# Kernel optimization log

Hardware: AMD Instinct MI355X
Metric: run time of the kernel (lower is better)

The kernel has to match this reference:

```python
import jax, jax.numpy as jnp
import numpy as np


def _inside_mask(points, boxes3d):
    # points: (B, N, 3); boxes3d: (B, M, 7) = (cx, cy, cz_bottom, dx, dy, dz, rz)
    cx, cy, cz, dx, dy, dz, rz = [boxes3d[..., i] for i in range(7)]
    cz = cz + dz * 0.5  # bottom-center -> geometric center (mmcv convention)
    # shift into box frame: (B, M, N)
    sx = points[:, None, :, 0] - cx[..., None]
    sy = points[:, None, :, 1] - cy[..., None]
    sz = points[:, None, :, 2] - cz[..., None]
    cosa = jnp.cos(-rz)[..., None]
    sina = jnp.sin(-rz)[..., None]
    lx = sx * cosa - sy * sina
    ly = sx * sina + sy * cosa
    return (
        (jnp.abs(lx) < dx[..., None] * 0.5)
        & (jnp.abs(ly) < dy[..., None] * 0.5)
        & (jnp.abs(sz) <= dz[..., None] * 0.5)
    )


def setup_inputs() -> dict:
    key = jax.random.key(0)
    k1, k2, k3 = jax.random.split(key, 3)
    B, N, M, C = 4, 16384, 128, 128
    points = jax.random.uniform(k1, (B, N, 3), dtype=jnp.float32)
    point_features = jax.random.normal(k2, (B, N, C), dtype=jnp.float32)
    boxes3d = jax.random.uniform(k3, (B, M, 7), dtype=jnp.float32)
    return {
        "points": points,
        "point_features": point_features,
        "boxes3d": boxes3d,
        "num_sampled_points": 512,
    }


def reference(points, point_features, boxes3d, num_sampled_points):
    S = num_sampled_points
    mask = _inside_mask(points, boxes3d)            # (B, M, N) bool
    cnt = mask.sum(axis=-1)                          # (B, M)
    # stable sort brings inside-point indices first, in original order
    order = jnp.argsort((~mask).astype(jnp.int32), axis=-1, stable=True)  # (B, M, N)
    cnt_safe = jnp.maximum(cnt, 1)
    # CUDA kernel: sample index k maps to k % cnt (== k when k < cnt)
    sample_pos = jnp.arange(S, dtype=cnt.dtype)[None, None, :] % cnt_safe[..., None]
    idx = jnp.take_along_axis(order, sample_pos, axis=-1)  # (B, M, S)
    gathered_pts = jnp.take_along_axis(points[:, None], idx[..., None], axis=2)          # (B, M, S, 3)
    gathered_feat = jnp.take_along_axis(point_features[:, None], idx[..., None], axis=2)  # (B, M, S, C)
    pooled = jnp.concatenate([gathered_pts, gathered_feat], axis=-1)  # (B, M, S, 3+C)
    nonempty = (cnt > 0)
    pooled = pooled * nonempty[..., None, None].astype(pooled.dtype)
    empty_flag = (~nonempty).astype(jnp.int32)
    return pooled, empty_flag
```

## Files before the change

kernel.cpp:

```cpp
#include <hip/hip_runtime.h>
#include <hip/hip_bf16.h>

#define BB   4
#define NN   16384
#define MM   128
#define CC   128
#define SS   512
#define CH   (CC + 3)
#define BM   (BB * MM)
#define WAVES 8
#define CHUNK (NN / WAVES)

__global__ __launch_bounds__(512)
void box_sample_kernel(const float* __restrict__ points,
                       const float* __restrict__ boxes,
                       int*  __restrict__ idx_ws,
                       int*  __restrict__ cnt_ws,
                       float* __restrict__ flag_out)
{
    const int box  = blockIdx.x;
    const int b    = box >> 7;
    const int lane = threadIdx.x & 63;
    const int w    = threadIdx.x >> 6;

    const float* P  = points + (size_t)b * NN * 3;
    const float* bx = boxes  + (size_t)box * 7;

    const float cx = bx[0], cy = bx[1], cz = bx[2];
    const float dx = bx[3], dy = bx[4], dz = bx[5], rz = bx[6];

    const float  czc = cz + dz * 0.5f;
    const float  hz  = dz * 0.5f;
    const double ca  = cos(-(double)rz);
    const double sa  = sin(-(double)rz);
    const double hx  = (double)dx * 0.5;
    const double hy  = (double)dy * 0.5;

    __shared__ int s_part[WAVES][SS];
    __shared__ int s_cnt[WAVES];
    __shared__ int s_idx[SS];

    int cnt = 0;
    const int pbase = w * CHUNK;
    for (int i0 = 0; i0 < CHUNK; i0 += 256) {
        float px[4], py[4], pz[4];
        #pragma unroll
        for (int u = 0; u < 4; ++u) {
            const int i = pbase + i0 + u * 64 + lane;
            px[u] = P[i * 3 + 0];
            py[u] = P[i * 3 + 1];
            pz[u] = P[i * 3 + 2];
        }
        #pragma unroll
        for (int u = 0; u < 4; ++u) {
            const double sx = (double)px[u] - (double)cx;
            const double sy = (double)py[u] - (double)cy;
            const float  szf = pz[u] - czc;
            const double lx = sx * ca - sy * sa;
            const double ly = sx * sa + sy * ca;
            const bool inside = (fabs(lx) < hx) && (fabs(ly) < hy) && (fabsf(szf) <= hz);
            const unsigned long long mask = __ballot(inside);
            const int pos = cnt + __popcll(mask & ((1ull << lane) - 1ull));
            if (inside && pos < SS) s_part[w][pos] = pbase + i0 + u * 64 + lane;
            cnt += __popcll(mask);
        }
    }
    if (lane == 0) s_cnt[w] = cnt;
    __syncthreads();

    int c[WAVES], off[WAVES];
    int total = 0;
    #pragma unroll
    for (int q = 0; q < WAVES; ++q) { c[q] = s_cnt[q]; off[q] = total; total += c[q]; }

    for (int k = threadIdx.x; k < SS; k += 512) {
        int v = 0;
        #pragma unroll
        for (int q = 0; q < WAVES; ++q) {
            const int r = k - off[q];
            if (r >= 0 && r < c[q]) v = s_part[q][r];
        }
        s_idx[k] = v;
    }
    __syncthreads();

    if (total > 0 && total < SS) {
        for (int k = total + threadIdx.x; k < SS; k += 512)
            s_idx[k] = s_idx[k % total];
        __syncthreads();
    }

    int* dst = idx_ws + (size_t)box * SS;
    for (int k = threadIdx.x; k < SS; k += 512) dst[k] = s_idx[k];
    if (threadIdx.x == 0) {
        cnt_ws[box]   = total;
        flag_out[box] = (total == 0) ? 1.0f : 0.0f;
    }
}

__global__ __launch_bounds__(256)
void gather_kernel(const float* __restrict__ points,
                   const float* __restrict__ feats,
                   const int*   __restrict__ idx_ws,
                   const int*   __restrict__ cnt_ws,
                   float* __restrict__ out)
{
    const int box   = blockIdx.x;
    const int chunk = blockIdx.y;
    const int b     = box >> 7;
    const int tid   = threadIdx.x;
    const int hw    = tid >> 5;
    const int j     = tid & 31;

    __shared__ int   s_idx[32];
    __shared__ float s_scale;
    __shared__ __align__(16) float s_buf[32 * CH];

    if (tid < 32) s_idx[tid] = idx_ws[(size_t)box * SS + chunk * 32 + tid];
    if (tid == 0) s_scale = (cnt_ws[box] > 0) ? 1.0f : 0.0f;
    __syncthreads();
    const float scale = s_scale;

    const float4* F4 = (const float4*)(feats + (size_t)b * NN * CC);
    const float*  Pb = points + (size_t)b * NN * 3;

    #pragma unroll
    for (int s = 0; s < 4; ++s) {
        const int k   = hw + s * 8;
        const int idx = s_idx[k];
        const float4 v = F4[idx * 32 + j];
        const int base = k * CH + 3 + 4 * j;
        s_buf[base + 0] = v.x * scale;
        s_buf[base + 1] = v.y * scale;
        s_buf[base + 2] = v.z * scale;
        s_buf[base + 3] = v.w * scale;
        if (j < 3) s_buf[k * CH + j] = Pb[idx * 3 + j] * scale;
    }
    __syncthreads();

    const float4* src4 = (const float4*)s_buf;
    float4* dst4 = (float4*)(out + (size_t)box * SS * CH + (size_t)chunk * 32 * CH);
    #pragma unroll
    for (int s = 0; s < 4; ++s) dst4[s * 256 + tid] = src4[s * 256 + tid];
    if (tid < 24) dst4[1024 + tid] = src4[1024 + tid];
}

extern "C" void kernel_launch(void* const* d_in, const int* in_sizes, int n_in,
                              void* d_out, int out_size, void* d_ws, size_t ws_size,
                              hipStream_t stream) {
    const float* points = (const float*)d_in[0];
    const float* feats  = (const float*)d_in[1];
    const float* boxes  = (const float*)d_in[2];

    int*  idx_ws = (int*)d_ws;
    int*  cnt_ws = idx_ws + (size_t)BM * SS;
    float* out      = (float*)d_out;
    float* flag_out = out + (size_t)BM * SS * CH;

    box_sample_kernel<<<BM, 512, 0, stream>>>(points, boxes, idx_ws, cnt_ws, flag_out);
    dim3 ggrid(BM, SS / 32);
    gather_kernel<<<ggrid, 256, 0, stream>>>(points, feats, idx_ws, cnt_ws, out);
}
```

Baseline: 197.7 us.

## Fuse box sampling and feature gather into one kernel per box

Merges the point-in-box sampling kernel and the gather kernel into a single kernel with one 512-thread block per box. The sampled indices stay in shared memory and the shared buffer is reused for staging 64 samples per iteration, so the index workspace round trip and the second launch go away. Output is written with nontemporal stores. In exchange the gather now runs with only 512 blocks and serialised per-box loops instead of 8192 blocks, which may reduce memory-level parallelism.

```diff
diff --git a/kernel.cpp b/kernel.cpp
--- a/kernel.cpp
+++ b/kernel.cpp
@@ -11,17 +11,20 @@
 #define WAVES 8
 #define CHUNK (NN / WAVES)
 
+typedef float vfloat4 __attribute__((ext_vector_type(4)));
+
 __global__ __launch_bounds__(512)
-void box_sample_kernel(const float* __restrict__ points,
-                       const float* __restrict__ boxes,
-                       int*  __restrict__ idx_ws,
-                       int*  __restrict__ cnt_ws,
-                       float* __restrict__ flag_out)
+void roipool_fused_kernel(const float* __restrict__ points,
+                          const float* __restrict__ feats,
+                          const float* __restrict__ boxes,
+                          float* __restrict__ out,
+                          float* __restrict__ flag_out)
 {
     const int box  = blockIdx.x;
     const int b    = box >> 7;
-    const int lane = threadIdx.x & 63;
-    const int w    = threadIdx.x >> 6;
+    const int tid  = threadIdx.x;
+    const int lane = tid & 63;
+    const int w    = tid >> 6;
 
     const float* P  = points + (size_t)b * NN * 3;
     const float* bx = boxes  + (size_t)box * 7;
@@ -36,9 +39,10 @@
     const double hx  = (double)dx * 0.5;
     const double hy  = (double)dy * 0.5;
 
-    __shared__ int s_part[WAVES][SS];
+    __shared__ __align__(16) float s_buf[64 * CH];
+    __shared__ int s_idx[SS];
     __shared__ int s_cnt[WAVES];
-    __shared__ int s_idx[SS];
+    int (*s_part)[SS] = (int (*)[SS])s_buf;
 
     int cnt = 0;
     const int pbase = w * CHUNK;
@@ -73,7 +77,7 @@
     #pragma unroll
     for (int q = 0; q < WAVES; ++q) { c[q] = s_cnt[q]; off[q] = total; total += c[q]; }
 
-    for (int k = threadIdx.x; k < SS; k += 512) {
+    for (int k = tid; k < SS; k += 512) {
         int v = 0;
         #pragma unroll
         for (int q = 0; q < WAVES; ++q) {
@@ -85,64 +89,44 @@
     __syncthreads();
 
     if (total > 0 && total < SS) {
-        for (int k = total + threadIdx.x; k < SS; k += 512)
+        for (int k = total + tid; k < SS; k += 512)
             s_idx[k] = s_idx[k % total];
-        __syncthreads();
-    }
-
-    int* dst = idx_ws + (size_t)box * SS;
-    for (int k = threadIdx.x; k < SS; k += 512) dst[k] = s_idx[k];
-    if (threadIdx.x == 0) {
-        cnt_ws[box]   = total;
-        flag_out[box] = (total == 0) ? 1.0f : 0.0f;
-    }
-}
-
-__global__ __launch_bounds__(256)
-void gather_kernel(const float* __restrict__ points,
-                   const float* __restrict__ feats,
-                   const int*   __restrict__ idx_ws,
-                   const int*   __restrict__ cnt_ws,
-                   float* __restrict__ out)
-{
-    const int box   = blockIdx.x;
-    const int chunk = blockIdx.y;
-    const int b     = box >> 7;
-    const int tid   = threadIdx.x;
-    const int hw    = tid >> 5;
-    const int j     = tid & 31;
-
-    __shared__ int   s_idx[32];
-    __shared__ float s_scale;
-    __shared__ __align__(16) float s_buf[32 * CH];
-
-    if (tid < 32) s_idx[tid] = idx_ws[(size_t)box * SS + chunk * 32 + tid];
-    if (tid == 0) s_scale = (cnt_ws[box] > 0) ? 1.0f : 0.0f;
-    __syncthreads();
-    const float scale = s_scale;
-
-    const float4* F4 = (const float4*)(feats + (size_t)b * NN * CC);
-    const float*  Pb = points + (size_t)b * NN * 3;
-
-    #pragma unroll
-    for (int s = 0; s < 4; ++s) {
-        const int k   = hw + s * 8;
-        const int idx = s_idx[k];
-        const float4 v = F4[idx * 32 + j];
-        const int base = k * CH + 3 + 4 * j;
-        s_buf[base + 0] = v.x * scale;
-        s_buf[base + 1] = v.y * scale;
-        s_buf[base + 2] = v.z * scale;
-        s_buf[base + 3] = v.w * scale;
-        if (j < 3) s_buf[k * CH + j] = Pb[idx * 3 + j] * scale;
     }
     __syncthreads();
 
-    const float4* src4 = (const float4*)s_buf;
-    float4* dst4 = (float4*)(out + (size_t)box * SS * CH + (size_t)chunk * 32 * CH);
-    #pragma unroll
-    for (int s = 0; s < 4; ++s) dst4[s * 256 + tid] = src4[s * 256 + tid];
-    if (tid < 24) dst4[1024 + tid] = src4[1024 + tid];
+    const float scale = (total > 0) ? 1.0f : 0.0f;
+    if (tid == 0) flag_out[box] = (total == 0) ? 1.0f : 0.0f;
+
+    const float4* F4 = (const float4*)(feats + (size_t)b * NN * CC);
+    const float*  Pb = P;
+    const int hw = tid >> 5;
+    const int j  = tid & 31;
+    float* outbox = out + (size_t)box * SS * CH;
+
+    for (int g = 0; g < 8; ++g) {
+        #pragma unroll
+        for (int s = 0; s < 4; ++s) {
+            const int kl  = s * 16 + hw;
+            const int idx = s_idx[g * 64 + kl];
+            const float4 v = F4[idx * 32 + j];
+            const int base = kl * CH + 3 + 4 * j;
+            s_buf[base + 0] = v.x * scale;
+            s_buf[base + 1] = v.y * scale;
+            s_buf[base + 2] = v.z * scale;
+            s_buf[base + 3] = v.w * scale;
+            if (j < 3) s_buf[kl * CH + j] = Pb[idx * 3 + j] * scale;
+        }
+        __syncthreads();
+
+        const vfloat4* src4 = (const vfloat4*)s_buf;
+        vfloat4* dst4 = (vfloat4*)(outbox + (size_t)g * 64 * CH);
+        #pragma unroll
+        for (int s = 0; s < 4; ++s)
+            __builtin_nontemporal_store(src4[s * 512 + tid], &dst4[s * 512 + tid]);
+        if (tid < 48)
+            __builtin_nontemporal_store(src4[2048 + tid], &dst4[2048 + tid]);
+        __syncthreads();
+    }
 }
 
 extern "C" void kernel_launch(void* const* d_in, const int* in_sizes, int n_in,
@@ -152,12 +136,8 @@
     const float* feats  = (const float*)d_in[1];
     const float* boxes  = (const float*)d_in[2];
 
-    int*  idx_ws = (int*)d_ws;
-    int*  cnt_ws = idx_ws + (size_t)BM * SS;
     float* out      = (float*)d_out;
     float* flag_out = out + (size_t)BM * SS * CH;
 
-    box_sample_kernel<<<BM, 512, 0, stream>>>(points, boxes, idx_ws, cnt_ws, flag_out);
-    dim3 ggrid(BM, SS / 32);
-    gather_kernel<<<ggrid, 256, 0, stream>>>(points, feats, idx_ws, cnt_ws, out);
+    roipool_fused_kernel<<<BM, 512, 0, stream>>>(points, feats, boxes, out, flag_out);
 }
```

Result: slower. 217.4 us (+10.0%).
